# Performance work log

Measured on AMD Instinct MI355X. Metric: run time of the kernel, lower is better.

## Reference

```python
import jax, jax.numpy as jnp
import numpy as np

NUM_NODES = 2048
NUM_OPS = 8
D, F, K = 64, 64, 64
H_NG = 128
H_EE = 64


def _make_edges(n):
    # edges[0]=i (src), edges[1]=j (dst) for i in [2,n), j in [0,i)
    src = np.concatenate([np.full(i, i, dtype=np.int64) for i in range(2, n)])
    dst = np.concatenate([np.arange(i, dtype=np.int64) for i in range(2, n)])
    return np.stack([src, dst])


def setup_inputs() -> dict:
    key = jax.random.key(0)
    ks = jax.random.split(key, 8)
    n = NUM_NODES
    s = lambda k, shape, fan_in: jax.random.normal(k, shape, jnp.float32) * (1.0 / np.sqrt(fan_in))
    return {
        "embed": jax.random.normal(ks[0], (n, D), jnp.float32),
        "W1": s(ks[1], (D, H_NG), D), "b1": jnp.zeros((H_NG,), jnp.float32),
        "W2": s(ks[2], (H_NG, H_NG), H_NG), "b2": jnp.zeros((H_NG,), jnp.float32),
        "W3": s(ks[3], (H_NG, F), H_NG), "b3": jnp.zeros((F,), jnp.float32),
        "We1": s(ks[4], (2 * F, H_EE), 2 * F), "be1": jnp.zeros((H_EE,), jnp.float32),
        "We2": s(ks[5], (H_EE, K), H_EE), "be2": jnp.zeros((K,), jnp.float32),
        "Wop": s(ks[6], (K, NUM_OPS), K), "bop": jnp.zeros((NUM_OPS,), jnp.float32),
        "edges": jnp.asarray(_make_edges(n)),
        "weights": jnp.ones((_make_edges(n).shape[1],), jnp.float32),
    }


def gcn_conv(x, W, b, src, dst, ew, n):
    # PyG GCNConv: x' = D^{-1/2} (A + I) D^{-1/2} (x W) + b, aggregated at dst
    h = x @ W
    loop = jnp.arange(n)
    src2 = jnp.concatenate([src, loop])
    dst2 = jnp.concatenate([dst, loop])
    w2 = jnp.concatenate([ew, jnp.ones((n,), x.dtype)])
    deg = jax.ops.segment_sum(w2, dst2, num_segments=n)
    dinv = jnp.where(deg > 0, jax.lax.rsqrt(deg), 0.0)
    norm = dinv[src2] * w2 * dinv[dst2]
    out = jax.ops.segment_sum(h[src2] * norm[:, None], dst2, num_segments=n)
    return out + b


def reference(embed, W1, b1, W2, b2, W3, b3, We1, be1, We2, be2, Wop, bop, edges, weights):
    n = embed.shape[0]
    src, dst = edges[0], edges[1]
    h = jax.nn.relu(gcn_conv(embed, W1, b1, src, dst, weights, n))
    h = jax.nn.relu(gcn_conv(h, W2, b2, src, dst, weights, n))
    h = jax.nn.relu(gcn_conv(h, W3, b3, src, dst, weights, n))  # [n, F]
    e = jnp.concatenate([h[src], h[dst]], axis=-1)              # [E, 2F]
    e = jax.nn.relu(e @ We1 + be1)
    e = jax.nn.relu(e @ We2 + be2)
    o = e @ Wop + bop                                            # [E, num_ops]
    p = jax.nn.softmax(o, axis=-1)
    # forward loop skips i == num_nodes-1; those rows of p remain zero
    mask = (src < n - 1)[:, None]
    return jnp.where(mask, p, 0.0)
```

## Files before the change

### kernel.cpp

```cpp
#include <hip/hip_runtime.h>
#include <math.h>

#define NN 2048
#define LASTN 2047

typedef __attribute__((ext_vector_type(8))) short short8;
typedef __attribute__((ext_vector_type(4))) float f32x4;
typedef __attribute__((ext_vector_type(4))) unsigned uint4v;

__device__ __forceinline__ float node_dinv(int j) {
  int deg = (j < 2) ? 2047 : (2048 - j);
  return rsqrtf((float)deg);
}

__device__ __forceinline__ void split_bf(float x, short& h, short& l) {
  unsigned u = __float_as_uint(x);
  unsigned r = u + 0x7FFFu + ((u >> 16) & 1u);
  h = (short)(r >> 16);
  float fh = __uint_as_float((r >> 16) << 16);
  float res = x - fh;
  unsigned u2 = __float_as_uint(res);
  unsigned r2 = u2 + 0x7FFFu + ((u2 >> 16) & 1u);
  l = (short)(r2 >> 16);
}

__device__ __forceinline__ unsigned cvt_pk_bf16(float a, float b) {
  unsigned r;
  asm("v_cvt_pk_bf16_f32 %0, %1, %2" : "=v"(r) : "v"(a), "v"(b));
  return r;
}

__device__ __forceinline__ void split_pair(float a, float b, unsigned& h, unsigned& l) {
  h = cvt_pk_bf16(a, b);
  float fa = __uint_as_float(h << 16);
  float fb = __uint_as_float(h & 0xFFFF0000u);
  l = cvt_pk_bf16(a - fa, b - fb);
}

__global__ __launch_bounds__(256) void prep(const float* __restrict__ embed,
                                            const float* __restrict__ We2,
                                            float* __restrict__ embedT,
                                            short* __restrict__ BfH,
                                            short* __restrict__ BfL) {
  __shared__ float tile[64][65];
  const int b = blockIdx.x;
  const int t = threadIdx.x;
  if (b < 32) {
    #pragma unroll
    for (int m = 0; m < 16; ++m) {
      int idx = m * 256 + t;
      int rl = idx >> 6, cc = idx & 63;
      tile[rl][cc] = embed[(b * 64 + rl) * 64 + cc];
    }
    __syncthreads();
    #pragma unroll
    for (int m = 0; m < 16; ++m) {
      int idx = m * 256 + t;
      int cc = idx >> 6, rl = idx & 63;
      embedT[cc * 2048 + b * 64 + rl] = tile[rl][cc];
    }
  } else {
    int tt = (b - 32) * 256 + t;
    int lane = tt & 63;
    int rest = tt >> 6;
    int ks = rest & 1;
    int ct = rest >> 1;
    int q = lane >> 4, l4 = lane & 15;
    int f = ct * 16 + l4;
    #pragma unroll
    for (int j = 0; j < 8; ++j) {
      int k = ks * 32 + q * 8 + j;
      float w = We2[k * 64 + f];
      short h, l;
      split_bf(w, h, l);
      int o = ((ct * 2 + ks) * 64 + lane) * 8 + j;
      BfH[o] = h;
      BfL[o] = l;
    }
  }
}

template <int K>
__global__ __launch_bounds__(512) void layer_fused(const float* __restrict__ XT,
                                                   const float* __restrict__ W,
                                                   const float* __restrict__ bias,
                                                   float* __restrict__ outT, int N) {
  const int c = blockIdx.x;
  const int t = threadIdx.x;
  __shared__ float wcol[K];
  __shared__ float part[2][512];
  if (t < K) wcol[t] = W[t * N + c];
  __syncthreads();
  float a0 = 0.f, a1 = 0.f, a2 = 0.f, a3 = 0.f;
  #pragma unroll 8
  for (int k = 0; k < K; ++k) {
    const float wk = wcol[k];
    const float4 x = *(const float4*)(XT + k * 2048 + 4 * t);
    a0 = fmaf(x.x, wk, a0);
    a1 = fmaf(x.y, wk, a1);
    a2 = fmaf(x.z, wk, a2);
    a3 = fmaf(x.w, wk, a3);
  }
  const int j0 = 4 * t;
  float s0 = a0 * node_dinv(j0);
  float s1 = a1 * node_dinv(j0 + 1);
  float s2 = a2 * node_dinv(j0 + 2);
  float s3 = a3 * node_dinv(j0 + 3);
  part[0][t] = (s0 + s1) + (s2 + s3);
  __syncthreads();
  int pb = 0;
  for (int off = 1; off < 512; off <<= 1) {
    part[pb ^ 1][t] = part[pb][t] + ((t + off < 512) ? part[pb][t + off] : 0.f);
    pb ^= 1;
    __syncthreads();
  }
  float Q = (t < 511) ? part[pb][t + 1] : 0.f;
  float Te3 = Q;
  float Te2 = Te3 + s3;
  float Te1 = Te2 + s2;
  float Te0 = Te1 + s1;
  const float bc = bias[c];
  float g0 = (j0 == 0) ? Te1 : Te0;
  float d0 = node_dinv(j0), d1 = node_dinv(j0 + 1);
  float d2 = node_dinv(j0 + 2), d3 = node_dinv(j0 + 3);
  float4 o;
  o.x = fmaxf(d0 * g0 + s0 * d0 + bc, 0.f);
  o.y = fmaxf(d1 * Te1 + s1 * d1 + bc, 0.f);
  o.z = fmaxf(d2 * Te2 + s2 * d2 + bc, 0.f);
  o.w = fmaxf(d3 * Te3 + s3 * d3 + bc, 0.f);
  *(float4*)(outT + (size_t)c * 2048 + j0) = o;
}

__global__ __launch_bounds__(256) void gemm_ab(const float* __restrict__ XT,
                                               const float* __restrict__ We1,
                                               const float* __restrict__ be1,
                                               float* __restrict__ A,
                                               float* __restrict__ B) {
  int idx = blockIdx.x * 256 + threadIdx.x;
  int r = idx >> 6, c = idx & 63;
  const float* WA = We1;
  const float* WB = We1 + 64 * 64;
  float a0 = 0.f, a1 = 0.f, b0 = 0.f, b1 = 0.f;
  for (int k = 0; k < 64; k += 2) {
    float x0 = XT[k * 2048 + r], x1 = XT[(k + 1) * 2048 + r];
    a0 = fmaf(x0, WA[k * 64 + c], a0);
    a1 = fmaf(x1, WA[(k + 1) * 64 + c], a1);
    b0 = fmaf(x0, WB[k * 64 + c], b0);
    b1 = fmaf(x1, WB[(k + 1) * 64 + c], b1);
  }
  A[idx] = a0 + a1 + be1[c];
  B[idx] = b0 + b1;
}

#define CHUNK 64
#define LSTR 68
#define EGY 2

__global__ __launch_bounds__(256, 4) void edge_mlp(const float* __restrict__ Amat,
                                                   const float* __restrict__ Bmat,
                                                   const short* __restrict__ BfH,
                                                   const short* __restrict__ BfL,
                                                   const float* __restrict__ be2,
                                                   const float* __restrict__ Wop,
                                                   const float* __restrict__ bop,
                                                   float* __restrict__ out) {
  const int i = LASTN - blockIdx.x;
  const long base = (long)i * (i - 1) / 2 - 1;
  const int tid = threadIdx.x;

  if (i == LASTN) {
    const float4 z = make_float4(0.f, 0.f, 0.f, 0.f);
    for (int j = blockIdx.y * 256 + tid; j < LASTN; j += EGY * 256) {
      size_t off = ((size_t)(base + j)) * 8;
      *(float4*)(out + off) = z;
      *(float4*)(out + off + 4) = z;
    }
    return;
  }

  int c = blockIdx.y;
  if (c * CHUNK >= i) return;

  __shared__ __align__(16) float sm[2][64 * LSTR];

  const int l = tid & 63, w = tid >> 6;
  const int l4 = l & 15, q = l >> 4;

  const float4* Arow = (const float4*)(Amat + (size_t)i * 64);
  const float4 a00 = Arow[q * 2], a01 = Arow[q * 2 + 1];
  const float4 a10 = Arow[8 + q * 2], a11 = Arow[8 + q * 2 + 1];

  short8 Bh[8], Bl[8];
  #pragma unroll
  for (int u = 0; u < 8; ++u) {
    Bh[u] = *(const short8*)(BfH + (u * 64 + l) * 8);
    Bl[u] = *(const short8*)(BfL + (u * 64 + l) * 8);
  }
  float bias[4];
  #pragma unroll
  for (int ct = 0; ct < 4; ++ct) bias[ct] = be2[ct * 16 + l4];

  auto stage_tile = [&](int cbase, int t, float* smb) {
    int j = cbase + t * 16 + l4;
    int jc = min(j, i - 1);
    const float4* Brow = (const float4*)(Bmat + (size_t)jc * 64);

    short8 ah[2], al[2];
    #pragma unroll
    for (int ks = 0; ks < 2; ++ks) {
      float4 bb0 = Brow[ks * 8 + q * 2];
      float4 bb1 = Brow[ks * 8 + q * 2 + 1];
      float4 aa0 = ks ? a10 : a00;
      float4 aa1 = ks ? a11 : a01;
      float v0 = fmaxf(aa0.x + bb0.x, 0.f), v1 = fmaxf(aa0.y + bb0.y, 0.f);
      float v2 = fmaxf(aa0.z + bb0.z, 0.f), v3 = fmaxf(aa0.w + bb0.w, 0.f);
      float v4 = fmaxf(aa1.x + bb1.x, 0.f), v5 = fmaxf(aa1.y + bb1.y, 0.f);
      float v6 = fmaxf(aa1.z + bb1.z, 0.f), v7 = fmaxf(aa1.w + bb1.w, 0.f);
      unsigned h0, h1, h2, h3, L0, L1, L2, L3;
      split_pair(v0, v1, h0, L0);
      split_pair(v2, v3, h1, L1);
      split_pair(v4, v5, h2, L2);
      split_pair(v6, v7, h3, L3);
      ah[ks] = __builtin_bit_cast(short8, (uint4v){h0, h1, h2, h3});
      al[ks] = __builtin_bit_cast(short8, (uint4v){L0, L1, L2, L3});
    }

    f32x4 acc[4];
    #pragma unroll
    for (int ct = 0; ct < 4; ++ct) acc[ct] = (f32x4){0.f, 0.f, 0.f, 0.f};
    #pragma unroll
    for (int ct = 0; ct < 4; ++ct)
      acc[ct] = __builtin_amdgcn_mfma_f32_16x16x32_bf16(ah[0], Bh[ct * 2 + 0], acc[ct], 0, 0, 0);
    #pragma unroll
    for (int ct = 0; ct < 4; ++ct)
      acc[ct] = __builtin_amdgcn_mfma_f32_16x16x32_bf16(ah[1], Bh[ct * 2 + 1], acc[ct], 0, 0, 0);
    #pragma unroll
    for (int ct = 0; ct < 4; ++ct)
      acc[ct] = __builtin_amdgcn_mfma_f32_16x16x32_bf16(ah[0], Bl[ct * 2 + 0], acc[ct], 0, 0, 0);
    #pragma unroll
    for (int ct = 0; ct < 4; ++ct)
      acc[ct] = __builtin_amdgcn_mfma_f32_16x16x32_bf16(ah[1], Bl[ct * 2 + 1], acc[ct], 0, 0, 0);
    #pragma unroll
    for (int ct = 0; ct < 4; ++ct)
      acc[ct] = __builtin_amdgcn_mfma_f32_16x16x32_bf16(al[0], Bh[ct * 2 + 0], acc[ct], 0, 0, 0);
    #pragma unroll
    for (int ct = 0; ct < 4; ++ct)
      acc[ct] = __builtin_amdgcn_mfma_f32_16x16x32_bf16(al[1], Bh[ct * 2 + 1], acc[ct], 0, 0, 0);

    #pragma unroll
    for (int ct = 0; ct < 4; ++ct) {
      float4 st;
      st.x = fmaxf(acc[ct][0] + bias[ct], 0.f);
      st.y = fmaxf(acc[ct][1] + bias[ct], 0.f);
      st.z = fmaxf(acc[ct][2] + bias[ct], 0.f);
      st.w = fmaxf(acc[ct][3] + bias[ct], 0.f);
      *(float4*)(&smb[(ct * 16 + l4) * LSTR + t * 16 + q * 4]) = st;
    }
  };

  auto phase_b = [&](int cbase, const float* smb) {
    int j = cbase + l;
    float o0 = bop[0], o1 = bop[1], o2 = bop[2], o3 = bop[3];
    float o4 = bop[4], o5 = bop[5], o6 = bop[6], o7 = bop[7];
    #pragma unroll 8
    for (int f = 0; f < 64; ++f) {
      float v = smb[f * LSTR + l];
      o0 = fmaf(v, Wop[f * 8 + 0], o0);
      o1 = fmaf(v, Wop[f * 8 + 1], o1);
      o2 = fmaf(v, Wop[f * 8 + 2], o2);
      o3 = fmaf(v, Wop[f * 8 + 3], o3);
      o4 = fmaf(v, Wop[f * 8 + 4], o4);
      o5 = fmaf(v, Wop[f * 8 + 5], o5);
      o6 = fmaf(v, Wop[f * 8 + 6], o6);
      o7 = fmaf(v, Wop[f * 8 + 7], o7);
    }
    float mx = fmaxf(fmaxf(fmaxf(o0, o1), fmaxf(o2, o3)),
                     fmaxf(fmaxf(o4, o5), fmaxf(o6, o7)));
    float p0 = __expf(o0 - mx), p1 = __expf(o1 - mx), p2 = __expf(o2 - mx);
    float p3 = __expf(o3 - mx), p4 = __expf(o4 - mx), p5 = __expf(o5 - mx);
    float p6 = __expf(o6 - mx), p7 = __expf(o7 - mx);
    float rs = 1.0f / (((p0 + p1) + (p2 + p3)) + ((p4 + p5) + (p6 + p7)));
    if (j < i) {
      size_t off = ((size_t)(base + j)) * 8;
      *(float4*)(out + off) = make_float4(p0 * rs, p1 * rs, p2 * rs, p3 * rs);
      *(float4*)(out + off + 4) = make_float4(p4 * rs, p5 * rs, p6 * rs, p7 * rs);
    }
  };

  stage_tile(c * CHUNK, w, sm[0]);
  __syncthreads();

  int buf = 0, kc = 0;
  while (true) {
    const int wb = kc & 3;
    const int nc = c + EGY;
    if (nc * CHUNK < i) {
      int rel = (w - wb) & 3;
      if (rel == 1) {
        stage_tile(nc * CHUNK, 0, sm[buf ^ 1]);
      } else if (rel == 2) {
        stage_tile(nc * CHUNK, 1, sm[buf ^ 1]);
        stage_tile(nc * CHUNK, 2, sm[buf ^ 1]);
      } else if (rel == 3) {
        stage_tile(nc * CHUNK, 3, sm[buf ^ 1]);
      }
    }
    if (w == wb) phase_b(c * CHUNK, sm[buf]);
    __syncthreads();
    c = nc;
    ++kc;
    buf ^= 1;
    if (c * CHUNK >= i) break;
  }
}

extern "C" void kernel_launch(void* const* d_in, const int* in_sizes, int n_in,
                              void* d_out, int out_size, void* d_ws, size_t ws_size,
                              hipStream_t stream) {
  const float* embed = (const float*)d_in[0];
  const float* W1 = (const float*)d_in[1];
  const float* b1 = (const float*)d_in[2];
  const float* W2 = (const float*)d_in[3];
  const float* b2 = (const float*)d_in[4];
  const float* W3 = (const float*)d_in[5];
  const float* b3 = (const float*)d_in[6];
  const float* We1 = (const float*)d_in[7];
  const float* be1 = (const float*)d_in[8];
  const float* We2 = (const float*)d_in[9];
  const float* be2 = (const float*)d_in[10];
  const float* Wop = (const float*)d_in[11];
  const float* bop = (const float*)d_in[12];

  float* ws = (float*)d_ws;
  float* embedT = ws;
  float* h2T = ws;
  float* h1T = ws + 262144;
  float* Abuf = ws + 262144;
  float* Bbuf = ws + 393216;
  float* h3T = ws + 524288;
  short* BfH = (short*)(ws + 655360);
  short* BfL = (short*)(ws + 657408);
  float* outp = (float*)d_out;

  prep<<<34, 256, 0, stream>>>(embed, We2, embedT, BfH, BfL);
  layer_fused<64><<<128, 512, 0, stream>>>(embedT, W1, b1, h1T, 128);
  layer_fused<128><<<128, 512, 0, stream>>>(h1T, W2, b2, h2T, 128);
  layer_fused<128><<<64, 512, 0, stream>>>(h2T, W3, b3, h3T, 64);
  gemm_ab<<<512, 256, 0, stream>>>(h3T, We1, be1, Abuf, Bbuf);

  dim3 ge(2046, EGY, 1);
  edge_mlp<<<ge, 256, 0, stream>>>(Abuf, Bbuf, BfH, BfL, be2, Wop, bop, outp);
}
```

Measured before the change: 251.3 us.

## Split softmax head across two waves with half-op lanes and rebalance staging

```diff
diff --git a/kernel.cpp b/kernel.cpp
--- a/kernel.cpp
+++ b/kernel.cpp
@@ -258,32 +258,33 @@
     }
   };
 
-  auto phase_b = [&](int cbase, const float* smb) {
-    int j = cbase + l;
-    float o0 = bop[0], o1 = bop[1], o2 = bop[2], o3 = bop[3];
-    float o4 = bop[4], o5 = bop[5], o6 = bop[6], o7 = bop[7];
+  auto phase_b_half = [&](int cbase, int bw, const float* smb) {
+    const int e = l & 31;
+    const int half = l >> 5;
+    const int ecol = bw * 32 + e;
+    const int j = cbase + ecol;
+    const float4 b4 = ((const float4*)bop)[half];
+    float o0 = b4.x, o1 = b4.y, o2 = b4.z, o3 = b4.w;
     #pragma unroll 8
     for (int f = 0; f < 64; ++f) {
-      float v = smb[f * LSTR + l];
-      o0 = fmaf(v, Wop[f * 8 + 0], o0);
-      o1 = fmaf(v, Wop[f * 8 + 1], o1);
-      o2 = fmaf(v, Wop[f * 8 + 2], o2);
-      o3 = fmaf(v, Wop[f * 8 + 3], o3);
-      o4 = fmaf(v, Wop[f * 8 + 4], o4);
-      o5 = fmaf(v, Wop[f * 8 + 5], o5);
-      o6 = fmaf(v, Wop[f * 8 + 6], o6);
-      o7 = fmaf(v, Wop[f * 8 + 7], o7);
-    }
-    float mx = fmaxf(fmaxf(fmaxf(o0, o1), fmaxf(o2, o3)),
-                     fmaxf(fmaxf(o4, o5), fmaxf(o6, o7)));
-    float p0 = __expf(o0 - mx), p1 = __expf(o1 - mx), p2 = __expf(o2 - mx);
-    float p3 = __expf(o3 - mx), p4 = __expf(o4 - mx), p5 = __expf(o5 - mx);
-    float p6 = __expf(o6 - mx), p7 = __expf(o7 - mx);
-    float rs = 1.0f / (((p0 + p1) + (p2 + p3)) + ((p4 + p5) + (p6 + p7)));
+      float v = smb[f * LSTR + ecol];
+      const float4 w4 = *(const float4*)(Wop + f * 8 + half * 4);
+      o0 = fmaf(v, w4.x, o0);
+      o1 = fmaf(v, w4.y, o1);
+      o2 = fmaf(v, w4.z, o2);
+      o3 = fmaf(v, w4.w, o3);
+    }
+    float own = fmaxf(fmaxf(o0, o1), fmaxf(o2, o3));
+    float oth = __shfl_xor(own, 32);
+    float mx = fmaxf(own, oth);
+    float p0 = __expf(o0 - mx), p1 = __expf(o1 - mx);
+    float p2 = __expf(o2 - mx), p3 = __expf(o3 - mx);
+    float s_own = (p0 + p1) + (p2 + p3);
+    float s_oth = __shfl_xor(s_own, 32);
+    float rs = 1.0f / (s_own + s_oth);
     if (j < i) {
-      size_t off = ((size_t)(base + j)) * 8;
-      *(float4*)(out + off) = make_float4(p0 * rs, p1 * rs, p2 * rs, p3 * rs);
-      *(float4*)(out + off + 4) = make_float4(p4 * rs, p5 * rs, p6 * rs, p7 * rs);
+      *(float4*)(out + ((size_t)(base + j)) * 8 + half * 4) =
+          make_float4(p0 * rs, p1 * rs, p2 * rs, p3 * rs);
     }
   };
 
@@ -292,20 +293,14 @@
 
   int buf = 0, kc = 0;
   while (true) {
-    const int wb = kc & 3;
+    const int bp = kc & 1;
     const int nc = c + EGY;
-    if (nc * CHUNK < i) {
-      int rel = (w - wb) & 3;
-      if (rel == 1) {
-        stage_tile(nc * CHUNK, 0, sm[buf ^ 1]);
-      } else if (rel == 2) {
-        stage_tile(nc * CHUNK, 1, sm[buf ^ 1]);
-        stage_tile(nc * CHUNK, 2, sm[buf ^ 1]);
-      } else if (rel == 3) {
-        stage_tile(nc * CHUNK, 3, sm[buf ^ 1]);
-      }
-    }
-    if (w == wb) phase_b(c * CHUNK, sm[buf]);
+    if ((w >> 1) == bp) {
+      phase_b_half(c * CHUNK, w & 1, sm[buf]);
+    } else if (nc * CHUNK < i) {
+      stage_tile(nc * CHUNK, (w & 1) * 2, sm[buf ^ 1]);
+      stage_tile(nc * CHUNK, (w & 1) * 2 + 1, sm[buf ^ 1]);
+    }
     __syncthreads();
     c = nc;
     ++kc;
```

Result: slower. 487.5 us (+94.0%).
